# Optimization experiments

Measured on AMD Instinct MI355X. Metric: run time of the kernel, lower is better.

Reference implementation:

```python
import jax, jax.numpy as jnp
import numpy as np

D_MODEL = 1024
NHEAD = 16
HEAD_DIM = D_MODEL // NHEAD
D_FF = 4096
EPS = 1e-5


def _layer_norm(x, gamma, beta):
    mu = jnp.mean(x, axis=-1, keepdims=True)
    var = jnp.mean((x - mu) ** 2, axis=-1, keepdims=True)
    return (x - mu) * jax.lax.rsqrt(var + EPS) * gamma + beta


def setup_inputs() -> dict:
    key = jax.random.key(0)
    ks = jax.random.split(key, 12)
    B, S = 2, 2048
    s = lambda fan_in: 1.0 / np.sqrt(fan_in)
    return {
        "src": jax.random.normal(ks[0], (B, S, D_MODEL), dtype=jnp.float32),
        "attn_bias": jax.random.normal(ks[1], (NHEAD, S, S), dtype=jnp.float32) * 0.02,
        "qkv_w": jax.random.uniform(ks[2], (3 * D_MODEL, D_MODEL), minval=-s(D_MODEL), maxval=s(D_MODEL)),
        "qkv_b": jax.random.uniform(ks[3], (3 * D_MODEL,), minval=-s(D_MODEL), maxval=s(D_MODEL)),
        "out_w": jax.random.uniform(ks[4], (D_MODEL, D_MODEL), minval=-s(D_MODEL), maxval=s(D_MODEL)),
        "out_b": jax.random.uniform(ks[5], (D_MODEL,), minval=-s(D_MODEL), maxval=s(D_MODEL)),
        "lin1_w": jax.random.uniform(ks[6], (D_FF, D_MODEL), minval=-s(D_MODEL), maxval=s(D_MODEL)),
        "lin1_b": jax.random.uniform(ks[7], (D_FF,), minval=-s(D_MODEL), maxval=s(D_MODEL)),
        "lin2_w": jax.random.uniform(ks[8], (D_MODEL, D_FF), minval=-s(D_FF), maxval=s(D_FF)),
        "lin2_b": jax.random.uniform(ks[9], (D_MODEL,), minval=-s(D_FF), maxval=s(D_FF)),
        "ln1_g": jnp.ones((D_MODEL,)), "ln1_b": jnp.zeros((D_MODEL,)),
        "ln2_g": jnp.ones((D_MODEL,)), "ln2_b": jnp.zeros((D_MODEL,)),
    }


def reference(src, attn_bias, qkv_w, qkv_b, out_w, out_b, lin1_w, lin1_b,
              lin2_w, lin2_b, ln1_g, ln1_b, ln2_g, ln2_b):
    B, S, _ = src.shape
    qkv = src @ qkv_w.T + qkv_b                      # [B,S,3D]
    q, k, v = jnp.split(qkv, 3, axis=-1)
    q = q.reshape(B, S, NHEAD, HEAD_DIM)
    k = k.reshape(B, S, NHEAD, HEAD_DIM)
    v = v.reshape(B, S, NHEAD, HEAD_DIM)
    scores = jnp.einsum('bthd,bshd->bhts', q, k) / np.sqrt(HEAD_DIM)
    scores = scores + attn_bias[None]                # 3D bias -> broadcast over batch
    weights = jax.nn.softmax(scores, axis=-1)
    ctx = jnp.einsum('bhts,bshd->bthd', weights, v).reshape(B, S, D_MODEL)
    attn_out = ctx @ out_w.T + out_b
    x = _layer_norm(src + attn_out, ln1_g, ln1_b)
    ff = jax.nn.gelu(x @ lin1_w.T + lin1_b, approximate=False) @ lin2_w.T + lin2_b
    return _layer_norm(x + ff, ln2_g, ln2_b)
```

## Files before the change

kernel.cpp:

```cpp
#include <hip/hip_runtime.h>
#include <hip/hip_bf16.h>


#define DMODEL 1024
#define NHEAD  16
#define HD     64
#define DFF    4096
#define SEQ    2048
#define BATCH  2
#define TOKD   ((size_t)4096 * 1024)

using short8 = __attribute__((ext_vector_type(8))) short;
using f32x4  = __attribute__((ext_vector_type(4))) float;
typedef unsigned short bfu;

__device__ __forceinline__ bfu f2bf(float f) {
    unsigned int u = __float_as_uint(f);
    unsigned int r = (u + 0x7fffu + ((u >> 16) & 1u)) >> 16;
    return (bfu)r;
}

__device__ __forceinline__ float gelu_exact(float x) {
    return 0.5f * x * (1.0f + erff(x * 0.70710678118654752f));
}

__device__ __forceinline__ void gload16(const void* g, void* l) {
    __builtin_amdgcn_global_load_lds(
        (const __attribute__((address_space(1))) void*)g,
        (__attribute__((address_space(3))) void*)l, 16, 0, 0);
}

__device__ __forceinline__ int swz(int row, int colbyte) {
    return (row * 128 + colbyte) ^ ((row & 7) << 4);
}

struct CvtPack {
    const float* in[5];
    bfu* out[5];
    unsigned start[6];
};

__global__ __launch_bounds__(256) void cvt_multi(CvtPack p) {
    unsigned gid = blockIdx.x * 256 + threadIdx.x;
    if (gid >= p.start[5]) return;
    int i = 0;
    #pragma unroll
    for (int k = 1; k < 5; ++k) i += (gid >= p.start[k]);
    unsigned local = gid - p.start[i];
    float4 v = *(const float4*)(p.in[i] + (size_t)local * 4);
    uint2 o;
    o.x = (unsigned)f2bf(v.x) | ((unsigned)f2bf(v.y) << 16);
    o.y = (unsigned)f2bf(v.z) | ((unsigned)f2bf(v.w) << 16);
    *(uint2*)(p.out[i] + (size_t)local * 4) = o;
}

template <int MODE, int BM, int SPLITK>
__global__ __launch_bounds__(256) void gemm_bt(const bfu* __restrict__ A,
                                               const bfu* __restrict__ W,
                                               const float* __restrict__ bias,
                                               void* __restrict__ Cout,
                                               int M, int N, int K) {
    constexpr int MR = BM / 32;
    __shared__ __align__(16) bfu As[2][BM * 32];
    __shared__ __align__(16) bfu Bs[2][128 * 32];
    const int tid = threadIdx.x;
    const int wid = tid >> 6, lane = tid & 63;
    const int lg = lane >> 4, li = lane & 15;

    const int nx = gridDim.x;
    int wg = blockIdx.x + nx * blockIdx.y;
    const int nwg = nx * gridDim.y;
    {
        const int qq = nwg >> 3, rr = nwg & 7;
        const int xcd = wg & 7, idx = wg >> 3;
        wg = (xcd < rr ? xcd * (qq + 1) : rr * (qq + 1) + (xcd - rr) * qq) + idx;
    }
    const int row0 = (wg % nx) * BM, col0 = (wg / nx) * 128;
    const int wr = (wid >> 1) * (BM / 2), wc = (wid & 1) * 64;
    f32x4 acc[MR][4] = {};

    const int kchunk = K / SPLITK;
    const int kbeg = blockIdx.z * kchunk;

    const int ch_row = tid >> 2;
    const int ch_col = (tid & 3) * 8;
    const bfu* Ag0 = A + (size_t)(row0 + ch_row) * K + kbeg + ch_col;
    const bfu* Ag1 = A + (size_t)(row0 + 64 + ch_row) * K + kbeg + ch_col;
    const bfu* Wg0 = W + (size_t)(col0 + ch_row) * K + kbeg + ch_col;
    const bfu* Wg1 = W + (size_t)(col0 + 64 + ch_row) * K + kbeg + ch_col;

    auto stage = [&](int buf, int k0) {
        gload16(Ag0 + k0, (char*)As[buf] + wid * 1024);
        if constexpr (BM == 128) gload16(Ag1 + k0, (char*)As[buf] + 4096 + wid * 1024);
        gload16(Wg0 + k0, (char*)Bs[buf] + wid * 1024);
        gload16(Wg1 + k0, (char*)Bs[buf] + 4096 + wid * 1024);
    };

    stage(0, 0);
    __syncthreads();
    int cur = 0;
    for (int k0 = 0; k0 < kchunk; k0 += 32) {
        if (k0 + 32 < kchunk) stage(cur ^ 1, k0 + 32);
        short8 af[MR], bf_[4];
        #pragma unroll
        for (int m = 0; m < MR; ++m)
            af[m] = *(const short8*)(As[cur] + (wr + m * 16 + li) * 32 + lg * 8);
        #pragma unroll
        for (int n = 0; n < 4; ++n)
            bf_[n] = *(const short8*)(Bs[cur] + (wc + n * 16 + li) * 32 + lg * 8);
        #pragma unroll
        for (int m = 0; m < MR; ++m)
            #pragma unroll
            for (int n = 0; n < 4; ++n)
                acc[m][n] = __builtin_amdgcn_mfma_f32_16x16x32_bf16(af[m], bf_[n], acc[m][n], 0, 0, 0);
        __syncthreads();
        cur ^= 1;
    }

    float* Cp3 = (float*)Cout + (size_t)blockIdx.z * M * N;
    #pragma unroll
    for (int m = 0; m < MR; ++m) {
        #pragma unroll
        for (int n = 0; n < 4; ++n) {
            #pragma unroll
            for (int r = 0; r < 4; ++r) {
                int row = row0 + wr + m * 16 + lg * 4 + r;
                int col = col0 + wc + n * 16 + li;
                if (MODE == 3) {
                    Cp3[(size_t)row * N + col] = acc[m][n][r];
                } else {
                    float v = acc[m][n][r] + bias[col];
                    if (MODE == 2) v = gelu_exact(v);
                    ((bfu*)Cout)[(size_t)row * N + col] = f2bf(v);
                }
            }
        }
    }
}

__global__ __launch_bounds__(256) void attn_kernel(const bfu* __restrict__ qkv,
                                                   const float* __restrict__ bias,
                                                   bfu* __restrict__ ctx) {
    __shared__ __align__(16) bfu Ks[128 * 64];
    __shared__ __align__(16) bfu Vt[2][64 * 64];
    __shared__ __align__(16) bfu Ps[4][16 * 64];
    const int tid = threadIdx.x;
    const int wid = tid >> 6, lane = tid & 63;
    const int lg = lane >> 4, li = lane & 15;
    const int q0 = blockIdx.x * 64;
    const int bh = blockIdx.y;
    const int h = bh >> 1, b = bh & 1;
    const size_t tokbase = (size_t)b * SEQ;

    short8 qa[2];
    {
        const bfu* qp = qkv + (tokbase + q0 + wid * 16 + li) * 3072 + h * 64;
        qa[0] = *(const short8*)(qp + lg * 8);
        qa[1] = *(const short8*)(qp + 32 + lg * 8);
    }

    f32x4 o[4] = {};
    float mrow[4], lrow[4];
    #pragma unroll
    for (int r = 0; r < 4; ++r) { mrow[r] = -1e30f; lrow[r] = 0.f; }

    char* pb = (char*)Ps[wid];
    const float* brow = bias + (size_t)h * SEQ * SEQ;
    const int qrbase = q0 + wid * 16 + lg * 4;

    const int krow  = tid >> 3;
    const int kcolb = (tid & 7) * 16;

    for (int kt = 0; kt < SEQ; kt += 128) {
        #pragma unroll
        for (int p = 0; p < 4; ++p) {
            int r_ = p * 32 + krow;
            uint4 v = *(const uint4*)(qkv + (tokbase + kt + r_) * 3072 + 1024 + h * 64 + (kcolb >> 1));
            *(uint4*)((char*)Ks + swz(r_, kcolb)) = v;
        }
        #pragma unroll
        for (int jh = 0; jh < 2; ++jh) {
            #pragma unroll
            for (int i = 0; i < 2; ++i) {
                int jb = i * 4 + wid;
                bfu tmp[8];
                #pragma unroll
                for (int u = 0; u < 8; ++u)
                    tmp[u] = qkv[(tokbase + kt + jh * 64 + jb * 8 + u) * 3072 + 2048 + h * 64 + lane];
                uint4 pv;
                pv.x = (unsigned)tmp[0] | ((unsigned)tmp[1] << 16);
                pv.y = (unsigned)tmp[2] | ((unsigned)tmp[3] << 16);
                pv.z = (unsigned)tmp[4] | ((unsigned)tmp[5] << 16);
                pv.w = (unsigned)tmp[6] | ((unsigned)tmp[7] << 16);
                *(uint4*)((char*)Vt[jh] + swz(lane, jb * 16)) = pv;
            }
        }

        float breg[4][8];
        #pragma unroll
        for (int r = 0; r < 4; ++r) {
            const float* bq = brow + (size_t)(qrbase + r) * SEQ + kt;
            #pragma unroll
            for (int nb = 0; nb < 8; ++nb)
                breg[r][nb] = bq[nb * 16 + li];
        }

        asm volatile("s_waitcnt lgkmcnt(0)" ::: "memory");
        __builtin_amdgcn_s_barrier();

        f32x4 s[8] = {};
        __builtin_amdgcn_s_setprio(1);
        #pragma unroll
        for (int cb = 0; cb < 2; ++cb) {
            #pragma unroll
            for (int nb = 0; nb < 8; ++nb) {
                short8 kf = *(const short8*)((char*)Ks + swz(nb * 16 + li, cb * 64 + lg * 16));
                s[nb] = __builtin_amdgcn_mfma_f32_16x16x32_bf16(qa[cb], kf, s[nb], 0, 0, 0);
            }
        }
        __builtin_amdgcn_s_setprio(0);

        #pragma unroll
        for (int r = 0; r < 4; ++r) {
            float sv[8];
            float mx = -1e30f;
            #pragma unroll
            for (int nb = 0; nb < 8; ++nb) {
                float v = s[nb][r] * 0.125f + breg[r][nb];
                sv[nb] = v;
                mx = fmaxf(mx, v);
            }
            #pragma unroll
            for (int off = 8; off; off >>= 1) mx = fmaxf(mx, __shfl_xor(mx, off));
            float mnew = fmaxf(mrow[r], mx);
            float sf = __expf(mrow[r] - mnew);
            mrow[r] = mnew;
            float rs = 0.f;
            #pragma unroll
            for (int nb = 0; nb < 8; ++nb) {
                float p = __expf(sv[nb] - mnew);
                rs += p;
                s[nb][r] = p;
            }
            #pragma unroll
            for (int off = 8; off; off >>= 1) rs += __shfl_xor(rs, off);
            lrow[r] = lrow[r] * sf + rs;
            #pragma unroll
            for (int dc = 0; dc < 4; ++dc) o[dc][r] *= sf;
        }

        #pragma unroll
        for (int jh = 0; jh < 2; ++jh) {
            #pragma unroll
            for (int nb = 0; nb < 4; ++nb)
                #pragma unroll
                for (int r = 0; r < 4; ++r)
                    *(bfu*)(pb + swz(lg * 4 + r, (nb * 16 + li) * 2)) =
                        (bfu)(__float_as_uint(s[jh * 4 + nb][r]) >> 16);
            __builtin_amdgcn_s_setprio(1);
            #pragma unroll
            for (int jb = 0; jb < 2; ++jb) {
                short8 pa = *(const short8*)(pb + swz(li, jb * 64 + lg * 16));
                short8 vb[4];
                #pragma unroll
                for (int dc = 0; dc < 4; ++dc)
                    vb[dc] = *(const short8*)((char*)Vt[jh] + swz(dc * 16 + li, jb * 64 + lg * 16));
                #pragma unroll
                for (int dc = 0; dc < 4; ++dc)
                    o[dc] = __builtin_amdgcn_mfma_f32_16x16x32_bf16(pa, vb[dc], o[dc], 0, 0, 0);
            }
            __builtin_amdgcn_s_setprio(0);
        }
        __syncthreads();
    }

    float il[4];
    #pragma unroll
    for (int r = 0; r < 4; ++r) il[r] = __builtin_amdgcn_rcpf(lrow[r]);
    #pragma unroll
    for (int dc = 0; dc < 4; ++dc)
        #pragma unroll
        for (int r = 0; r < 4; ++r) {
            int qr = qrbase + r;
            int d = dc * 16 + li;
            float v = o[dc][r] * il[r];
            ctx[(tokbase + qr) * 1024 + h * 64 + d] = f2bf(v);
        }
}

template <int P, bool ABF>
__global__ __launch_bounds__(256) void residual_lnP(const void* __restrict__ a,
                                                    const float* __restrict__ parts,
                                                    const float* __restrict__ pbias,
                                                    const float* __restrict__ g,
                                                    const float* __restrict__ be,
                                                    float* __restrict__ xf,
                                                    bfu* __restrict__ xb) {
    const int row = blockIdx.x, t = threadIdx.x;
    const size_t off = (size_t)row * DMODEL + t * 4;
    float4 v;
    if constexpr (ABF) {
        uint2 u = *(const uint2*)((const bfu*)a + off);
        v.x = __uint_as_float((u.x & 0xffffu) << 16);
        v.y = __uint_as_float(u.x & 0xffff0000u);
        v.z = __uint_as_float((u.y & 0xffffu) << 16);
        v.w = __uint_as_float(u.y & 0xffff0000u);
    } else {
        v = *(const float4*)((const float*)a + off);
    }
    #pragma unroll
    for (int i = 0; i < P; ++i) {
        float4 p = *(const float4*)(parts + i * TOKD + off);
        v.x += p.x; v.y += p.y; v.z += p.z; v.w += p.w;
    }
    float4 pb = *(const float4*)(pbias + t * 4);
    v.x += pb.x; v.y += pb.y; v.z += pb.z; v.w += pb.w;

    float s  = v.x + v.y + v.z + v.w;
    float sq = v.x * v.x + v.y * v.y + v.z * v.z + v.w * v.w;
    #pragma unroll
    for (int o2 = 32; o2; o2 >>= 1) { s += __shfl_xor(s, o2); sq += __shfl_xor(sq, o2); }
    __shared__ float red[8];
    const int wid = t >> 6, lane = t & 63;
    if (lane == 0) { red[wid] = s; red[4 + wid] = sq; }
    __syncthreads();
    s  = red[0] + red[1] + red[2] + red[3];
    sq = red[4] + red[5] + red[6] + red[7];
    float mu  = s * (1.0f / DMODEL);
    float var = sq * (1.0f / DMODEL) - mu * mu;
    float rstd = rsqrtf(var + 1e-5f);
    float4 gv  = *(const float4*)(g + t * 4);
    float4 bev = *(const float4*)(be + t * 4);
    float4 ov;
    ov.x = (v.x - mu) * rstd * gv.x + bev.x;
    ov.y = (v.y - mu) * rstd * gv.y + bev.y;
    ov.z = (v.z - mu) * rstd * gv.z + bev.z;
    ov.w = (v.w - mu) * rstd * gv.w + bev.w;
    if (xf) *(float4*)(xf + off) = ov;
    if (xb) {
        uint2 o;
        o.x = (unsigned)f2bf(ov.x) | ((unsigned)f2bf(ov.y) << 16);
        o.y = (unsigned)f2bf(ov.z) | ((unsigned)f2bf(ov.w) << 16);
        *(uint2*)(xb + off) = o;
    }
}

extern "C" void kernel_launch(void* const* d_in, const int* in_sizes, int n_in,
                              void* d_out, int out_size, void* d_ws, size_t ws_size,
                              hipStream_t stream) {
    const float* src    = (const float*)d_in[0];
    const float* abias  = (const float*)d_in[1];
    const float* qkv_w  = (const float*)d_in[2];
    const float* qkv_b  = (const float*)d_in[3];
    const float* out_w  = (const float*)d_in[4];
    const float* out_b  = (const float*)d_in[5];
    const float* lin1_w = (const float*)d_in[6];
    const float* lin1_b = (const float*)d_in[7];
    const float* lin2_w = (const float*)d_in[8];
    const float* lin2_b = (const float*)d_in[9];
    const float* ln1_g  = (const float*)d_in[10];
    const float* ln1_b  = (const float*)d_in[11];
    const float* ln2_g  = (const float*)d_in[12];
    const float* ln2_b  = (const float*)d_in[13];
    float* out = (float*)d_out;

    const int T = BATCH * SEQ;
    char* w = (char*)d_ws;
    auto take = [&](size_t bytes) { char* p = w; w += (bytes + 255) & ~(size_t)255; return p; };
    bfu*   src_bf  = (bfu*)take((size_t)T * DMODEL * 2);
    bfu*   qkvw_bf = (bfu*)take((size_t)3 * DMODEL * DMODEL * 2);
    bfu*   outw_bf = (bfu*)take((size_t)DMODEL * DMODEL * 2);
    bfu*   l1w_bf  = (bfu*)take((size_t)DFF * DMODEL * 2);
    bfu*   l2w_bf  = (bfu*)take((size_t)DMODEL * DFF * 2);
    bfu*   qkv_bf  = (bfu*)take((size_t)T * 3 * DMODEL * 2);
    bfu*   ctx_bf  = (bfu*)take((size_t)T * DMODEL * 2);
    float* outp_p  = (float*)take((size_t)2 * T * DMODEL * 4);
    bfu*   x_bf    = (bfu*)take((size_t)T * DMODEL * 2);
    bfu*   h1_bf   = (bfu*)take((size_t)T * DFF * 2);
    float* l2_p    = (float*)take((size_t)2 * T * DMODEL * 4);

    {
        CvtPack p;
        p.in[0] = src;    p.out[0] = src_bf;
        p.in[1] = qkv_w;  p.out[1] = qkvw_bf;
        p.in[2] = out_w;  p.out[2] = outw_bf;
        p.in[3] = lin1_w; p.out[3] = l1w_bf;
        p.in[4] = lin2_w; p.out[4] = l2w_bf;
        unsigned n4[5] = {
            (unsigned)((size_t)T * DMODEL / 4),
            (unsigned)((size_t)3 * DMODEL * DMODEL / 4),
            (unsigned)((size_t)DMODEL * DMODEL / 4),
            (unsigned)((size_t)DFF * DMODEL / 4),
            (unsigned)((size_t)DMODEL * DFF / 4)};
        p.start[0] = 0;
        for (int i = 0; i < 5; ++i) p.start[i + 1] = p.start[i] + n4[i];
        cvt_multi<<<(p.start[5] + 255) / 256, 256, 0, stream>>>(p);
    }

    gemm_bt<0, 128, 1><<<dim3(T / 128, (3 * DMODEL) / 128, 1), 256, 0, stream>>>(
        src_bf, qkvw_bf, qkv_b, qkv_bf, T, 3 * DMODEL, DMODEL);
    attn_kernel<<<dim3(SEQ / 64, BATCH * NHEAD), 256, 0, stream>>>(qkv_bf, abias, ctx_bf);
    gemm_bt<3, 64, 2><<<dim3(T / 64, DMODEL / 128, 2), 256, 0, stream>>>(
        ctx_bf, outw_bf, nullptr, outp_p, T, DMODEL, DMODEL);
    residual_lnP<2, false><<<T, 256, 0, stream>>>(src, outp_p, out_b, ln1_g, ln1_b,
                                                  nullptr, x_bf);
    gemm_bt<2, 128, 1><<<dim3(T / 128, DFF / 128, 1), 256, 0, stream>>>(
        x_bf, l1w_bf, lin1_b, h1_bf, T, DFF, DMODEL);
    gemm_bt<3, 64, 2><<<dim3(T / 64, DMODEL / 128, 2), 256, 0, stream>>>(
        h1_bf, l2w_bf, nullptr, l2_p, T, DMODEL, DFF);
    residual_lnP<2, true><<<T, 256, 0, stream>>>(x_bf, l2_p, lin2_b, ln2_g, ln2_b,
                                                 out, nullptr);
}
```

Before: 353.9 us.

## Pre-transpose V and double-buffer K/V tiles with async global-to-LDS loads

Adds a separate kernel that transposes V into a per-head [d][seq] layout, so the attention kernel no longer gathers V with strided scalar loads. The attention kernel now double-buffers K and V tiles in LDS, using direct global-to-LDS loads (gload16) for the next tile while computing the current one, and synchronises with vmcnt waits. This costs an extra kernel launch, an extra pass over V in global memory, and twice the LDS footprint, which may reduce occupancy. The hand-tuned vmcnt counts are fragile.

```diff
diff --git a/kernel.cpp b/kernel.cpp
--- a/kernel.cpp
+++ b/kernel.cpp
@@ -52,6 +52,38 @@
     o.x = (unsigned)f2bf(v.x) | ((unsigned)f2bf(v.y) << 16);
     o.y = (unsigned)f2bf(v.z) | ((unsigned)f2bf(v.w) << 16);
     *(uint2*)(p.out[i] + (size_t)local * 4) = o;
+}
+
+__global__ __launch_bounds__(256) void vtrans_kernel(const bfu* __restrict__ qkv,
+                                                     bfu* __restrict__ vt) {
+    __shared__ bfu Ld[64][72];
+    const int s0 = blockIdx.x * 64;
+    const int bh = blockIdx.y;
+    const int b = bh >> 4, h = bh & 15;
+    const int tid = threadIdx.x;
+    const int r = tid >> 2, c = (tid & 3) * 16;
+    const bfu* src = qkv + ((size_t)(b * SEQ + s0 + r)) * 3072 + 2048 + h * 64 + c;
+    uint4 v0 = *(const uint4*)(src);
+    uint4 v1 = *(const uint4*)(src + 8);
+    *(uint4*)&Ld[r][c] = v0;
+    *(uint4*)&Ld[r][c + 8] = v1;
+    __syncthreads();
+    const int d = tid >> 2, sc = (tid & 3) * 16;
+    bfu tmp[16];
+    #pragma unroll
+    for (int u = 0; u < 16; ++u) tmp[u] = Ld[sc + u][d];
+    uint4 o0, o1;
+    o0.x = (unsigned)tmp[0] | ((unsigned)tmp[1] << 16);
+    o0.y = (unsigned)tmp[2] | ((unsigned)tmp[3] << 16);
+    o0.z = (unsigned)tmp[4] | ((unsigned)tmp[5] << 16);
+    o0.w = (unsigned)tmp[6] | ((unsigned)tmp[7] << 16);
+    o1.x = (unsigned)tmp[8] | ((unsigned)tmp[9] << 16);
+    o1.y = (unsigned)tmp[10] | ((unsigned)tmp[11] << 16);
+    o1.z = (unsigned)tmp[12] | ((unsigned)tmp[13] << 16);
+    o1.w = (unsigned)tmp[14] | ((unsigned)tmp[15] << 16);
+    bfu* dst = vt + ((size_t)bh * 64 + d) * 2048 + s0 + sc;
+    *(uint4*)(dst) = o0;
+    *(uint4*)(dst + 8) = o1;
 }
 
 template <int MODE, int BM, int SPLITK>
@@ -139,10 +171,11 @@
 }
 
 __global__ __launch_bounds__(256) void attn_kernel(const bfu* __restrict__ qkv,
+                                                   const bfu* __restrict__ vt,
                                                    const float* __restrict__ bias,
                                                    bfu* __restrict__ ctx) {
-    __shared__ __align__(16) bfu Ks[128 * 64];
-    __shared__ __align__(16) bfu Vt[2][64 * 64];
+    __shared__ __align__(16) bfu Ks[2][128 * 64];
+    __shared__ __align__(16) bfu Vs[2][2 * 64 * 64];
     __shared__ __align__(16) bfu Ps[4][16 * 64];
     const int tid = threadIdx.x;
     const int wid = tid >> 6, lane = tid & 63;
@@ -168,33 +201,29 @@
     const float* brow = bias + (size_t)h * SEQ * SEQ;
     const int qrbase = q0 + wid * 16 + lg * 4;
 
-    const int krow  = tid >> 3;
-    const int kcolb = (tid & 7) * 16;
-
+    const int sr  = tid >> 3;
+    const int scs = (((tid & 7) * 16) ^ ((sr & 7) << 4)) >> 1;
+    const size_t vbase = ((size_t)(b * 16 + h) * 64) * 2048;
+
+    auto stageK = [&](int buf, int kt) {
+        #pragma unroll
+        for (int p = 0; p < 4; ++p)
+            gload16(qkv + (size_t)(tokbase + kt + p * 32 + sr) * 3072 + 1024 + h * 64 + scs,
+                    (char*)Ks[buf] + p * 4096 + wid * 1024);
+    };
+    auto stageV = [&](int buf, int kt) {
+        #pragma unroll
+        for (int p = 0; p < 4; ++p)
+            gload16(vt + vbase + (size_t)((p & 1) * 32 + sr) * 2048 + kt + (p >> 1) * 64 + scs,
+                    (char*)Vs[buf] + p * 4096 + wid * 1024);
+    };
+
+    stageK(0, 0);
+    stageV(0, 0);
+
+    int cur = 0;
     for (int kt = 0; kt < SEQ; kt += 128) {
-        #pragma unroll
-        for (int p = 0; p < 4; ++p) {
-            int r_ = p * 32 + krow;
-            uint4 v = *(const uint4*)(qkv + (tokbase + kt + r_) * 3072 + 1024 + h * 64 + (kcolb >> 1));
-            *(uint4*)((char*)Ks + swz(r_, kcolb)) = v;
-        }
-        #pragma unroll
-        for (int jh = 0; jh < 2; ++jh) {
-            #pragma unroll
-            for (int i = 0; i < 2; ++i) {
-                int jb = i * 4 + wid;
-                bfu tmp[8];
-                #pragma unroll
-                for (int u = 0; u < 8; ++u)
-                    tmp[u] = qkv[(tokbase + kt + jh * 64 + jb * 8 + u) * 3072 + 2048 + h * 64 + lane];
-                uint4 pv;
-                pv.x = (unsigned)tmp[0] | ((unsigned)tmp[1] << 16);
-                pv.y = (unsigned)tmp[2] | ((unsigned)tmp[3] << 16);
-                pv.z = (unsigned)tmp[4] | ((unsigned)tmp[5] << 16);
-                pv.w = (unsigned)tmp[6] | ((unsigned)tmp[7] << 16);
-                *(uint4*)((char*)Vt[jh] + swz(lane, jb * 16)) = pv;
-            }
-        }
+        const int ktn = (kt + 128 < SEQ) ? kt + 128 : 0;
 
         float breg[4][8];
         #pragma unroll
@@ -204,21 +233,28 @@
             for (int nb = 0; nb < 8; ++nb)
                 breg[r][nb] = bq[nb * 16 + li];
         }
-
-        asm volatile("s_waitcnt lgkmcnt(0)" ::: "memory");
+        asm volatile("" ::: "memory");
+
+        stageK(cur ^ 1, ktn);
+        stageV(cur ^ 1, ktn);
+
+        asm volatile("s_waitcnt vmcnt(40)" ::: "memory");
         __builtin_amdgcn_s_barrier();
 
         f32x4 s[8] = {};
+        const char* Kb = (const char*)Ks[cur];
         __builtin_amdgcn_s_setprio(1);
         #pragma unroll
         for (int cb = 0; cb < 2; ++cb) {
             #pragma unroll
             for (int nb = 0; nb < 8; ++nb) {
-                short8 kf = *(const short8*)((char*)Ks + swz(nb * 16 + li, cb * 64 + lg * 16));
+                short8 kf = *(const short8*)(Kb + swz(nb * 16 + li, cb * 64 + lg * 16));
                 s[nb] = __builtin_amdgcn_mfma_f32_16x16x32_bf16(qa[cb], kf, s[nb], 0, 0, 0);
             }
         }
         __builtin_amdgcn_s_setprio(0);
+
+        asm volatile("s_waitcnt vmcnt(8)" ::: "memory");
 
         #pragma unroll
         for (int r = 0; r < 4; ++r) {
@@ -249,6 +285,7 @@
             for (int dc = 0; dc < 4; ++dc) o[dc][r] *= sf;
         }
 
+        const char* Vb = (const char*)Vs[cur];
         #pragma unroll
         for (int jh = 0; jh < 2; ++jh) {
             #pragma unroll
@@ -264,14 +301,15 @@
                 short8 vb[4];
                 #pragma unroll
                 for (int dc = 0; dc < 4; ++dc)
-                    vb[dc] = *(const short8*)((char*)Vt[jh] + swz(dc * 16 + li, jb * 64 + lg * 16));
+                    vb[dc] = *(const short8*)(Vb + jh * 8192 + swz(dc * 16 + li, jb * 64 + lg * 16));
                 #pragma unroll
                 for (int dc = 0; dc < 4; ++dc)
                     o[dc] = __builtin_amdgcn_mfma_f32_16x16x32_bf16(pa, vb[dc], o[dc], 0, 0, 0);
             }
             __builtin_amdgcn_s_setprio(0);
         }
-        __syncthreads();
+        __builtin_amdgcn_s_barrier();
+        cur ^= 1;
     }
 
     float il[4];
@@ -373,6 +411,7 @@
     bfu*   l1w_bf  = (bfu*)take((size_t)DFF * DMODEL * 2);
     bfu*   l2w_bf  = (bfu*)take((size_t)DMODEL * DFF * 2);
     bfu*   qkv_bf  = (bfu*)take((size_t)T * 3 * DMODEL * 2);
+    bfu*   vt_bf   = (bfu*)take((size_t)T * DMODEL * 2);
     bfu*   ctx_bf  = (bfu*)take((size_t)T * DMODEL * 2);
     float* outp_p  = (float*)take((size_t)2 * T * DMODEL * 4);
     bfu*   x_bf    = (bfu*)take((size_t)T * DMODEL * 2);
@@ -399,7 +438,8 @@
 
     gemm_bt<0, 128, 1><<<dim3(T / 128, (3 * DMODEL) / 128, 1), 256, 0, stream>>>(
         src_bf, qkvw_bf, qkv_b, qkv_bf, T, 3 * DMODEL, DMODEL);
-    attn_kernel<<<dim3(SEQ / 64, BATCH * NHEAD), 256, 0, stream>>>(qkv_bf, abias, ctx_bf);
+    vtrans_kernel<<<dim3(SEQ / 64, BATCH * NHEAD), 256, 0, stream>>>(qkv_bf, vt_bf);
+    attn_kernel<<<dim3(SEQ / 64, BATCH * NHEAD), 256, 0, stream>>>(qkv_bf, vt_bf, abias, ctx_bf);
     gemm_bt<3, 64, 2><<<dim3(T / 64, DMODEL / 128, 2), 256, 0, stream>>>(
         ctx_bf, outw_bf, nullptr, outp_p, T, DMODEL, DMODEL);
     residual_lnP<2, false><<<T, 256, 0, stream>>>(src, outp_p, out_b, ln1_g, ln1_b,
```

Measured after the change: 361.9 us. 1.02x slower.

## Transpose QK^T MFMA so each lane owns one query row in softmax

Applied to the files above, without the earlier changes.

Swaps the MFMA operands for the score computation so each lane holds 32 scores of a single query row instead of 4 rows. This lets the attention bias load as contiguous float4 vectors per row and cuts the online softmax to one running max/sum per lane with two cross-lane shuffles instead of four rows of four-step reductions. Rescale factors and final normalizers are gathered back to the output layout with shuffles, and the P tile is written to LDS in transposed order. The transposed LDS stores may add bank conflicts.

```diff
diff --git a/kernel.cpp b/kernel.cpp
--- a/kernel.cpp
+++ b/kernel.cpp
@@ -160,13 +160,13 @@
     }
 
     f32x4 o[4] = {};
-    float mrow[4], lrow[4];
-    #pragma unroll
-    for (int r = 0; r < 4; ++r) { mrow[r] = -1e30f; lrow[r] = 0.f; }
+    float m_ = -1e30f, l_ = 0.f;
 
     char* pb = (char*)Ps[wid];
     const float* brow = bias + (size_t)h * SEQ * SEQ;
+    const int qlane  = q0 + wid * 16 + li;
     const int qrbase = q0 + wid * 16 + lg * 4;
+    const int srcb = (lane & 48) | (((lane >> 4) & 3) << 2);
 
     const int krow  = tid >> 3;
     const int kcolb = (tid & 7) * 16;
@@ -196,14 +196,10 @@
             }
         }
 
-        float breg[4][8];
-        #pragma unroll
-        for (int r = 0; r < 4; ++r) {
-            const float* bq = brow + (size_t)(qrbase + r) * SEQ + kt;
-            #pragma unroll
-            for (int nb = 0; nb < 8; ++nb)
-                breg[r][nb] = bq[nb * 16 + li];
-        }
+        float4 bb[8];
+        #pragma unroll
+        for (int f = 0; f < 8; ++f)
+            bb[f] = *(const float4*)(brow + (size_t)qlane * SEQ + kt + f * 16 + lg * 4);
 
         asm volatile("s_waitcnt lgkmcnt(0)" ::: "memory");
         __builtin_amdgcn_s_barrier();
@@ -215,39 +211,47 @@
             #pragma unroll
             for (int nb = 0; nb < 8; ++nb) {
                 short8 kf = *(const short8*)((char*)Ks + swz(nb * 16 + li, cb * 64 + lg * 16));
-                s[nb] = __builtin_amdgcn_mfma_f32_16x16x32_bf16(qa[cb], kf, s[nb], 0, 0, 0);
+                s[nb] = __builtin_amdgcn_mfma_f32_16x16x32_bf16(kf, qa[cb], s[nb], 0, 0, 0);
             }
         }
         __builtin_amdgcn_s_setprio(0);
 
-        #pragma unroll
-        for (int r = 0; r < 4; ++r) {
-            float sv[8];
-            float mx = -1e30f;
-            #pragma unroll
-            for (int nb = 0; nb < 8; ++nb) {
-                float v = s[nb][r] * 0.125f + breg[r][nb];
-                sv[nb] = v;
+        float mx = -1e30f;
+        #pragma unroll
+        for (int f = 0; f < 8; ++f) {
+            #pragma unroll
+            for (int r = 0; r < 4; ++r) {
+                float v = s[f][r] * 0.125f + ((const float*)&bb[f])[r];
+                s[f][r] = v;
                 mx = fmaxf(mx, v);
             }
-            #pragma unroll
-            for (int off = 8; off; off >>= 1) mx = fmaxf(mx, __shfl_xor(mx, off));
-            float mnew = fmaxf(mrow[r], mx);
-            float sf = __expf(mrow[r] - mnew);
-            mrow[r] = mnew;
-            float rs = 0.f;
-            #pragma unroll
-            for (int nb = 0; nb < 8; ++nb) {
-                float p = __expf(sv[nb] - mnew);
+        }
+        mx = fmaxf(mx, __shfl_xor(mx, 16));
+        mx = fmaxf(mx, __shfl_xor(mx, 32));
+        float mnew = fmaxf(m_, mx);
+        float sf_ = __expf(m_ - mnew);
+        m_ = mnew;
+        float rs = 0.f;
+        #pragma unroll
+        for (int f = 0; f < 8; ++f) {
+            #pragma unroll
+            for (int r = 0; r < 4; ++r) {
+                float p = __expf(s[f][r] - mnew);
                 rs += p;
-                s[nb][r] = p;
-            }
-            #pragma unroll
-            for (int off = 8; off; off >>= 1) rs += __shfl_xor(rs, off);
-            lrow[r] = lrow[r] * sf + rs;
-            #pragma unroll
-            for (int dc = 0; dc < 4; ++dc) o[dc][r] *= sf;
-        }
+                s[f][r] = p;
+            }
+        }
+        rs += __shfl_xor(rs, 16);
+        rs += __shfl_xor(rs, 32);
+        l_ = l_ * sf_ + rs;
+
+        float sfq[4];
+        #pragma unroll
+        for (int r = 0; r < 4; ++r) sfq[r] = __shfl(sf_, srcb + r);
+        #pragma unroll
+        for (int dc = 0; dc < 4; ++dc)
+            #pragma unroll
+            for (int r = 0; r < 4; ++r) o[dc][r] *= sfq[r];
 
         #pragma unroll
         for (int jh = 0; jh < 2; ++jh) {
@@ -255,7 +259,7 @@
             for (int nb = 0; nb < 4; ++nb)
                 #pragma unroll
                 for (int r = 0; r < 4; ++r)
-                    *(bfu*)(pb + swz(lg * 4 + r, (nb * 16 + li) * 2)) =
+                    *(bfu*)(pb + swz(li, (nb * 16 + lg * 4 + r) * 2)) =
                         (bfu)(__float_as_uint(s[jh * 4 + nb][r]) >> 16);
             __builtin_amdgcn_s_setprio(1);
             #pragma unroll
@@ -276,7 +280,7 @@
 
     float il[4];
     #pragma unroll
-    for (int r = 0; r < 4; ++r) il[r] = __builtin_amdgcn_rcpf(lrow[r]);
+    for (int r = 0; r < 4; ++r) il[r] = __builtin_amdgcn_rcpf(__shfl(l_, srcb + r));
     #pragma unroll
     for (int dc = 0; dc < 4; ++dc)
         #pragma unroll
```

Measured after the change: 349.0 us (median of 2 runs). No clear change (-1.4%).
